# Optimization experiments

Measured on AMD Instinct MI355X. Metric: run time of the kernel, lower is better.

Reference implementation:

```python
import jax, jax.numpy as jnp
import numpy as np

N, E, IN = 90000, 540000, 30
H1, H2, H3, H4 = 128, 128, 128, 64

def _glorot(k, i, o):
    return jax.random.normal(k, (i, o), jnp.float32) * np.float32(np.sqrt(2.0 / (i + o)))

def setup_inputs() -> dict:
    key = jax.random.key(0)
    ks = jax.random.split(key, 20)
    inp = {
        'x': jax.random.normal(ks[0], (N, IN), jnp.float32),
        'edge_index': jax.random.randint(ks[1], (2, E), 0, N, dtype=jnp.int32),
    }
    shapes = [(IN, H1), (H1, H2), (H2, H3), (H3, H4)]
    i = 2
    for br in ('s', 't'):
        for li, (din, dout) in enumerate(shapes, start=1):
            inp[f'w{li}{br}'] = _glorot(ks[i], din, dout); i += 1
            inp[f'b{li}{br}'] = jnp.zeros((dout,), jnp.float32)
    return inp

def _mlp(h, w1, b1, w2, b2):
    # Linear -> (Dropout eval = identity) -> ReLU -> Linear
    return jax.nn.relu(h @ w1 + b1) @ w2 + b2

def _gin(h, src, dst, w1, b1, w2, b2):
    # GINConv with eps=0: MLP(x_i + sum_{j->i} x_j)
    agg = jax.ops.segment_sum(h[src], dst, num_segments=N)
    return _mlp(h + agg, w1, b1, w2, b2)

def reference(x, edge_index, w1s, b1s, w2s, b2s, w3s, b3s, w4s, b4s,
              w1t, b1t, w2t, b2t, w3t, b3t, w4t, b4t):
    src, dst = edge_index[0], edge_index[1]
    z_src = _gin(x, src, dst, w1s, b1s, w2s, b2s)       # [N, H2]
    z_src = _gin(z_src, src, dst, w3s, b3s, w4s, b4s)   # [N, H4]
    z_tar = _gin(x, src, dst, w1t, b1t, w2t, b2t)
    z_tar = _gin(z_tar, src, dst, w3t, b3t, w4t, b4t)
    zs = z_src.reshape(-1, 9, H4)  # [G, 9, H4]
    zt = z_tar.reshape(-1, 9, H4)
    adj = jnp.einsum('gik,gjk->gij', zs, zt)  # per-graph 9x9 matmul
    return adj.reshape(-1, 9)  # [N, 9], matches torch.cat along dim 0
```

## Files before the change

kernel.cpp:

```cpp
#include <hip/hip_runtime.h>
#include <hip/hip_bf16.h>


typedef __attribute__((ext_vector_type(8))) short short8;
typedef __attribute__((ext_vector_type(4))) float f32x4;

#define MAXDEG 64

__device__ inline unsigned short f2bf(float f) {
    union { float f; unsigned u; } v; v.f = f;
    unsigned r = v.u + 0x7fffu + ((v.u >> 16) & 1u);
    return (unsigned short)(r >> 16);
}
__device__ inline float bflo(unsigned u) { return __uint_as_float(u << 16); }
__device__ inline float bfhi(unsigned u) { return __uint_as_float(u & 0xffff0000u); }
__device__ inline unsigned packbf(float a, float b) {
    return (unsigned)f2bf(a) | ((unsigned)f2bf(b) << 16);
}

#define W1S_OFF 0
#define W2S_OFF 4096
#define W3S_OFF 20480
#define W4S_OFF 36864
#define W1T_OFF 45056
#define W2T_OFF 49152
#define W3T_OFF 65536
#define W4T_OFF 81920
#define PACK_USHORTS 90112
#define WPACK_BLOCKS 176

__global__ __launch_bounds__(256) void prep_bucket_kernel(
    const float* w0, const float* w1, const float* w2, const float* w3,
    const float* w4, const float* w5, const float* w6, const float* w7,
    unsigned short* __restrict__ pack,
    const float* __restrict__ x, float* __restrict__ xpad,
    const int* __restrict__ src, const int* __restrict__ dst,
    int* __restrict__ deg, int* __restrict__ colb,
    int N, int E, int nbE)
{
    int bid = blockIdx.x;
    if (bid < nbE) {
        int e = bid * 256 + threadIdx.x;
        if (e < E) {
            int d = dst[e];
            int slot = atomicAdd(&deg[d], 1);
            if (slot < MAXDEG) colb[(size_t)d * MAXDEG + slot] = src[e];
        }
        return;
    }
    bid -= nbE;
    if (bid < WPACK_BLOCKS) {
        if (threadIdx.x >= 64) return;
        const int prefix[9] = {0, 8, 40, 72, 88, 96, 128, 160, 176};
        const int KTa[8] = {1, 4, 4, 4, 1, 4, 4, 4};
        const int KRa[8] = {30, 128, 128, 128, 30, 128, 128, 128};
        const int Ca[8]  = {128, 128, 128, 64, 128, 128, 128, 64};
        const int DOFF[8] = {W1S_OFF, W2S_OFF, W3S_OFF, W4S_OFF,
                             W1T_OFF, W2T_OFF, W3T_OFF, W4T_OFF};
        const float* Ws[8] = {w0, w1, w2, w3, w4, w5, w6, w7};
        int mi = 0;
        while (mi < 7 && bid >= prefix[mi + 1]) ++mi;
        int lt = bid - prefix[mi];
        int kt = lt % KTa[mi], ct = lt / KTa[mi];
        const float* W = Ws[mi];
        int l = threadIdx.x;
        int n = ct * 16 + (l & 15);
        for (int j = 0; j < 8; ++j) {
            int k = kt * 32 + (l >> 4) * 8 + j;
            float v = (k < KRa[mi]) ? W[(size_t)k * Ca[mi] + n] : 0.f;
            pack[(size_t)DOFF[mi] + (size_t)lt * 512 + l * 8 + j] = f2bf(v);
        }
    } else {
        int gid = (bid - WPACK_BLOCKS) * 256 + threadIdx.x;
        if (gid >= N * 32) return;
        int n = gid >> 5, f = gid & 31;
        xpad[gid] = (f < 30) ? x[(size_t)n * 30 + f] : 0.f;
    }
}

__global__ __launch_bounds__(512, 8) void mlp1_kernel(
    const float* __restrict__ xpad, const int* __restrict__ deg,
    const int* __restrict__ colb, const unsigned short* __restrict__ pack,
    const float* __restrict__ b1s, const float* __restrict__ b2s,
    const float* __restrict__ b1t, const float* __restrict__ b2t,
    unsigned short* __restrict__ z1cat, int N)
{
    __shared__ __align__(16) unsigned short hs[64 * 40];
    __shared__ __align__(16) unsigned short hm[2][64 * 136];
    const int tid = threadIdx.x;
    const int n0blk = blockIdx.x * 64;

    {
        const int row = tid >> 3, l = tid & 7;
        int gn = n0blk + row;
        float4 a = {0.f, 0.f, 0.f, 0.f};
        if (gn < N) {
            const float4* base = (const float4*)xpad;
            a = base[(size_t)gn * 8 + l];
            const int* col = colb + (size_t)gn * MAXDEG;
            int e = min(deg[gn], MAXDEG);
            int i = 0;
            for (; i + 4 <= e; i += 4) {
                int s0 = col[i], s1 = col[i + 1], s2 = col[i + 2], s3 = col[i + 3];
                float4 v0 = base[(size_t)s0 * 8 + l];
                float4 v1 = base[(size_t)s1 * 8 + l];
                float4 v2 = base[(size_t)s2 * 8 + l];
                float4 v3 = base[(size_t)s3 * 8 + l];
                a.x += v0.x; a.y += v0.y; a.z += v0.z; a.w += v0.w;
                a.x += v1.x; a.y += v1.y; a.z += v1.z; a.w += v1.w;
                a.x += v2.x; a.y += v2.y; a.z += v2.z; a.w += v2.w;
                a.x += v3.x; a.y += v3.y; a.z += v3.z; a.w += v3.w;
            }
            for (; i + 2 <= e; i += 2) {
                int s0 = col[i], s1 = col[i + 1];
                float4 v0 = base[(size_t)s0 * 8 + l];
                float4 v1 = base[(size_t)s1 * 8 + l];
                a.x += v0.x; a.y += v0.y; a.z += v0.z; a.w += v0.w;
                a.x += v1.x; a.y += v1.y; a.z += v1.z; a.w += v1.w;
            }
            for (; i < e; ++i) {
                float4 v0 = base[(size_t)col[i] * 8 + l];
                a.x += v0.x; a.y += v0.y; a.z += v0.z; a.w += v0.w;
            }
        }
        uint2 o; o.x = packbf(a.x, a.y); o.y = packbf(a.z, a.w);
        *(uint2*)&hs[row * 40 + l * 4] = o;
    }
    __syncthreads();

    const int half = tid >> 8;
    const int ltid = tid & 255;
    const int wv = ltid >> 6, l = ltid & 63, q = l >> 4, m = l & 15;
    const float* B1 = half ? b1t : b1s;
    const float* B2 = half ? b2t : b2s;
    const int w1off = half ? W1T_OFF : W1S_OFF;
    const int w2off = half ? W2T_OFF : W2S_OFF;
    unsigned short* hmb = hm[half];

    {
        short8 a[4];
        #pragma unroll
        for (int nt = 0; nt < 4; ++nt)
            a[nt] = *(const short8*)&hs[(nt * 16 + m) * 40 + q * 8];
        #pragma unroll
        for (int ci = 0; ci < 2; ++ci) {
            int ct = wv * 2 + ci;
            short8 bf = *(const short8*)&pack[w1off + ((size_t)ct * 64 + l) * 8];
            float bias = B1[ct * 16 + m];
            #pragma unroll
            for (int nt = 0; nt < 4; ++nt) {
                f32x4 acc = {0.f, 0.f, 0.f, 0.f};
                acc = __builtin_amdgcn_mfma_f32_16x16x32_bf16(a[nt], bf, acc, 0, 0, 0);
                #pragma unroll
                for (int r = 0; r < 4; ++r) {
                    float v = fmaxf(acc[r] + bias, 0.f);
                    hmb[(nt * 16 + q * 4 + r) * 136 + ct * 16 + m] = f2bf(v);
                }
            }
        }
    }
    __syncthreads();

    f32x4 acc2[4][2];
    #pragma unroll
    for (int nt = 0; nt < 4; ++nt)
        #pragma unroll
        for (int ci = 0; ci < 2; ++ci)
            acc2[nt][ci] = (f32x4){0.f, 0.f, 0.f, 0.f};
    for (int nt = 0; nt < 4; ++nt) {
        short8 a[4];
        #pragma unroll
        for (int kt = 0; kt < 4; ++kt)
            a[kt] = *(const short8*)&hmb[(nt * 16 + m) * 136 + kt * 32 + q * 8];
        #pragma unroll
        for (int ci = 0; ci < 2; ++ci) {
            int ct = wv * 2 + ci;
            #pragma unroll
            for (int kt = 0; kt < 4; ++kt) {
                short8 bf = *(const short8*)&pack[w2off + ((size_t)(ct * 4 + kt) * 64 + l) * 8];
                acc2[nt][ci] = __builtin_amdgcn_mfma_f32_16x16x32_bf16(a[kt], bf, acc2[nt][ci], 0, 0, 0);
            }
        }
    }
    __syncthreads();
    #pragma unroll
    for (int ci = 0; ci < 2; ++ci) {
        int ct = wv * 2 + ci;
        float bias = B2[ct * 16 + m];
        #pragma unroll
        for (int nt = 0; nt < 4; ++nt)
            #pragma unroll
            for (int r = 0; r < 4; ++r)
                hmb[(nt * 16 + q * 4 + r) * 136 + ct * 16 + m] =
                    f2bf(acc2[nt][ci][r] + bias);
    }
    __syncthreads();
    for (int c = tid; c < 2048; c += 512) {
        int row = c >> 5, off = c & 31;
        int gn = n0blk + row;
        if (gn < N) {
            short8 v = *(const short8*)&hm[off >> 4][row * 136 + (off & 15) * 8];
            *(short8*)&z1cat[(size_t)gn * 256 + off * 8] = v;
        }
    }
}

__global__ __launch_bounds__(512, 8) void mlp2_kernel(
    const unsigned short* __restrict__ z1, const int* __restrict__ deg,
    const int* __restrict__ colb, const unsigned short* __restrict__ pack,
    const float* __restrict__ b3s, const float* __restrict__ b4s,
    const float* __restrict__ b3t, const float* __restrict__ b4t,
    float* __restrict__ out, int N, int G)
{
    __shared__ __align__(16) unsigned short hs[36 * 264];
    __shared__ __align__(16) unsigned short hm[36 * 136];
    float* hsf = (float*)hs;
    const int tid = threadIdx.x;
    const int n0blk = blockIdx.x * 36;
    const int wv = tid >> 6, l = tid & 63;

    {
        const uint2* b2 = (const uint2*)z1;
        for (int rr = 0; rr < 5; ++rr) {
            int row = wv + rr * 8;
            if (row >= 36) break;
            int gn = n0blk + row;
            float a0 = 0.f, a1 = 0.f, a2 = 0.f, a3 = 0.f;
            if (gn < N) {
                uint2 s = b2[(size_t)gn * 64 + l];
                a0 = bflo(s.x); a1 = bfhi(s.x); a2 = bflo(s.y); a3 = bfhi(s.y);
                const int* col = colb + (size_t)gn * MAXDEG;
                int e = min(deg[gn], MAXDEG);
                #pragma unroll
                for (int i = 0; i < 8; ++i) {
                    int valid = i < e;
                    int s0 = valid ? col[i] : gn;
                    float fv = valid ? 1.f : 0.f;
                    uint2 v = b2[(size_t)s0 * 64 + l];
                    a0 = fmaf(fv, bflo(v.x), a0);
                    a1 = fmaf(fv, bfhi(v.x), a1);
                    a2 = fmaf(fv, bflo(v.y), a2);
                    a3 = fmaf(fv, bfhi(v.y), a3);
                }
                int i = 8;
                for (; i + 4 <= e; i += 4) {
                    int s0 = col[i], s1 = col[i + 1], s2 = col[i + 2], s3 = col[i + 3];
                    uint2 v0 = b2[(size_t)s0 * 64 + l];
                    uint2 v1 = b2[(size_t)s1 * 64 + l];
                    uint2 v2 = b2[(size_t)s2 * 64 + l];
                    uint2 v3 = b2[(size_t)s3 * 64 + l];
                    a0 += bflo(v0.x); a1 += bfhi(v0.x); a2 += bflo(v0.y); a3 += bfhi(v0.y);
                    a0 += bflo(v1.x); a1 += bfhi(v1.x); a2 += bflo(v1.y); a3 += bfhi(v1.y);
                    a0 += bflo(v2.x); a1 += bfhi(v2.x); a2 += bflo(v2.y); a3 += bfhi(v2.y);
                    a0 += bflo(v3.x); a1 += bfhi(v3.x); a2 += bflo(v3.y); a3 += bfhi(v3.y);
                }
                for (; i < e; ++i) {
                    uint2 v0 = b2[(size_t)col[i] * 64 + l];
                    a0 += bflo(v0.x); a1 += bfhi(v0.x); a2 += bflo(v0.y); a3 += bfhi(v0.y);
                }
            }
            uint2 o; o.x = packbf(a0, a1); o.y = packbf(a2, a3);
            *(uint2*)&hs[row * 264 + l * 4] = o;
        }
    }
    __syncthreads();

    const int q = l >> 4, m = l & 15;

    for (int br = 0; br < 2; ++br) {
        const int w1off = br ? W3T_OFF : W3S_OFF;
        const int w2off = br ? W4T_OFF : W4S_OFF;
        const float* B1 = br ? b3t : b3s;
        const float* B2 = br ? b4t : b4s;
        if (br) __syncthreads();

        #pragma unroll
        for (int ti = 0; ti < 3; ++ti) {
            const int tile = wv * 3 + ti;
            const int ct = tile & 7;
            const int nt = tile >> 3;
            const int ar = min(nt * 16 + m, 35);
            float bias = B1[ct * 16 + m];
            short8 a[4];
            #pragma unroll
            for (int kt = 0; kt < 4; ++kt)
                a[kt] = *(const short8*)&hs[ar * 264 + br * 128 + kt * 32 + q * 8];
            f32x4 acc = {0.f, 0.f, 0.f, 0.f};
            #pragma unroll
            for (int kt = 0; kt < 4; ++kt) {
                short8 bf = *(const short8*)&pack[w1off + ((size_t)(ct * 4 + kt) * 64 + l) * 8];
                acc = __builtin_amdgcn_mfma_f32_16x16x32_bf16(a[kt], bf, acc, 0, 0, 0);
            }
            #pragma unroll
            for (int r = 0; r < 4; ++r) {
                int hrow = nt * 16 + q * 4 + r;
                if (hrow < 36) {
                    float v = fmaxf(acc[r] + bias, 0.f);
                    hm[hrow * 136 + ct * 16 + m] = f2bf(v);
                }
            }
        }
        __syncthreads();

        #pragma unroll
        for (int ti = 0; ti < 2; ++ti) {
            const int tile = ti * 8 + wv;
            if (tile < 12) {
                const int ct = tile & 3;
                const int nt = tile >> 2;
                const int ar = min(nt * 16 + m, 35);
                float bias = B2[ct * 16 + m];
                short8 a[4];
                #pragma unroll
                for (int kt = 0; kt < 4; ++kt)
                    a[kt] = *(const short8*)&hm[ar * 136 + kt * 32 + q * 8];
                f32x4 acc = {0.f, 0.f, 0.f, 0.f};
                #pragma unroll
                for (int kt = 0; kt < 4; ++kt) {
                    short8 bf = *(const short8*)&pack[w2off + ((size_t)(ct * 4 + kt) * 64 + l) * 8];
                    acc = __builtin_amdgcn_mfma_f32_16x16x32_bf16(a[kt], bf, acc, 0, 0, 0);
                }
                #pragma unroll
                for (int r = 0; r < 4; ++r) {
                    int zrow = nt * 16 + q * 4 + r;
                    if (zrow < 36)
                        hsf[zrow * 132 + br * 64 + ct * 16 + m] = acc[r] + bias;
                }
            }
        }
    }
    __syncthreads();

    if (tid < 324) {
        int gl = tid / 81, rem = tid - gl * 81;
        int i = rem / 9, j = rem - i * 9;
        int g = blockIdx.x * 4 + gl;
        if (g < G) {
            const float* srow = &hsf[(gl * 9 + i) * 132];
            const float* trow = &hsf[(gl * 9 + j) * 132 + 64];
            float acc = 0.f;
            #pragma unroll
            for (int k = 0; k < 64; ++k) acc += srow[k] * trow[k];
            out[(size_t)g * 81 + i * 9 + j] = acc;
        }
    }
}

extern "C" void kernel_launch(void* const* d_in, const int* in_sizes, int n_in,
                              void* d_out, int out_size, void* d_ws, size_t ws_size,
                              hipStream_t stream)
{
    const float* x  = (const float*)d_in[0];
    const int*   ei = (const int*)d_in[1];
    const int N_ = in_sizes[0] / 30;
    const int E_ = in_sizes[1] / 2;
    const int* src = ei;
    const int* dst = ei + E_;

    const float* w1s = (const float*)d_in[2];
    const float* b1s = (const float*)d_in[3];
    const float* w2s = (const float*)d_in[4];
    const float* b2s = (const float*)d_in[5];
    const float* w3s = (const float*)d_in[6];
    const float* b3s = (const float*)d_in[7];
    const float* w4s = (const float*)d_in[8];
    const float* b4s = (const float*)d_in[9];
    const float* w1t = (const float*)d_in[10];
    const float* b1t = (const float*)d_in[11];
    const float* w2t = (const float*)d_in[12];
    const float* b2t = (const float*)d_in[13];
    const float* w3t = (const float*)d_in[14];
    const float* b3t = (const float*)d_in[15];
    const float* w4t = (const float*)d_in[16];
    const float* b4t = (const float*)d_in[17];

    int* deg  = (int*)d_ws;
    int* colb = deg + N_;
    size_t int_bytes = ((size_t)N_ * (1 + MAXDEG)) * sizeof(int);
    size_t pb = (int_bytes + 15) & ~(size_t)15;
    unsigned short* packu = (unsigned short*)((char*)d_ws + pb);
    float* xpad = (float*)(packu + PACK_USHORTS);
    unsigned short* z1cat = (unsigned short*)(xpad + (size_t)N_ * 32);
    size_t need = pb + (size_t)PACK_USHORTS * 2
                + (size_t)N_ * 32 * 4
                + (size_t)N_ * 256 * 2;
    if (ws_size < need) return;

    const int nbE  = (E_ + 255) / 256;
    const int nb64 = (N_ + 63) / 64;
    const int nb36 = (N_ + 35) / 36;
    const int nbX  = (N_ * 32 + 255) / 256;

    hipMemsetAsync(deg, 0, (size_t)N_ * sizeof(int), stream);

    prep_bucket_kernel<<<nbE + WPACK_BLOCKS + nbX, 256, 0, stream>>>(
        w1s, w2s, w3s, w4s, w1t, w2t, w3t, w4t, packu, x, xpad,
        src, dst, deg, colb, N_, E_, nbE);

    mlp1_kernel<<<nb64, 512, 0, stream>>>(xpad, deg, colb, packu,
        b1s, b2s, b1t, b2t, z1cat, N_);

    mlp2_kernel<<<nb36, 512, 0, stream>>>(z1cat, deg, colb, packu,
        b3s, b4s, b3t, b4t, (float*)d_out, N_, N_ / 9);
}
```

Baseline: 248.1 us.

## Stage neighbor row gathers through LDS with double-buffered async global_load_lds

Replaces the per-lane register gather of neighbor feature rows in the second-layer aggregation with a double-buffered staging scheme. Each wave fetches four neighbor rows at a time directly into a private LDS slice with global_load_lds, prefetching the next chunk while summing the current one. The staging area is carved out of an enlarged shared buffer that also hosts the hm array, so per-block LDS grows and occupancy may drop. The code has no explicit wait on the async copies before reading LDS, so correctness relies on waits the compiler inserts.

```diff
diff --git a/kernel.cpp b/kernel.cpp
--- a/kernel.cpp
+++ b/kernel.cpp
@@ -212,14 +212,18 @@
     const float* __restrict__ b3t, const float* __restrict__ b4t,
     float* __restrict__ out, int N, int G)
 {
-    __shared__ __align__(16) unsigned short hs[36 * 264];
-    __shared__ __align__(16) unsigned short hm[36 * 136];
-    float* hsf = (float*)hs;
+    __shared__ __align__(16) unsigned char smem[19008 + 32768];
+    unsigned short* hs = (unsigned short*)smem;
+    unsigned short* hm = (unsigned short*)(smem + 19008);
+    unsigned char*  stg = smem + 19008;
+    float* hsf = (float*)smem;
     const int tid = threadIdx.x;
     const int n0blk = blockIdx.x * 36;
     const int wv = tid >> 6, l = tid & 63;
 
     {
+        unsigned char* mystg = stg + wv * 4096;
+        const int hl = l >> 5, ll = l & 31;
         const uint2* b2 = (const uint2*)z1;
         for (int rr = 0; rr < 5; ++rr) {
             int row = wv + rr * 8;
@@ -231,32 +235,43 @@
                 a0 = bflo(s.x); a1 = bfhi(s.x); a2 = bflo(s.y); a3 = bfhi(s.y);
                 const int* col = colb + (size_t)gn * MAXDEG;
                 int e = min(deg[gn], MAXDEG);
-                #pragma unroll
-                for (int i = 0; i < 8; ++i) {
-                    int valid = i < e;
-                    int s0 = valid ? col[i] : gn;
-                    float fv = valid ? 1.f : 0.f;
-                    uint2 v = b2[(size_t)s0 * 64 + l];
-                    a0 = fmaf(fv, bflo(v.x), a0);
-                    a1 = fmaf(fv, bfhi(v.x), a1);
-                    a2 = fmaf(fv, bflo(v.y), a2);
-                    a3 = fmaf(fv, bfhi(v.y), a3);
-                }
-                int i = 8;
-                for (; i + 4 <= e; i += 4) {
-                    int s0 = col[i], s1 = col[i + 1], s2 = col[i + 2], s3 = col[i + 3];
-                    uint2 v0 = b2[(size_t)s0 * 64 + l];
-                    uint2 v1 = b2[(size_t)s1 * 64 + l];
-                    uint2 v2 = b2[(size_t)s2 * 64 + l];
-                    uint2 v3 = b2[(size_t)s3 * 64 + l];
-                    a0 += bflo(v0.x); a1 += bfhi(v0.x); a2 += bflo(v0.y); a3 += bfhi(v0.y);
-                    a0 += bflo(v1.x); a1 += bfhi(v1.x); a2 += bflo(v1.y); a3 += bfhi(v1.y);
-                    a0 += bflo(v2.x); a1 += bfhi(v2.x); a2 += bflo(v2.y); a3 += bfhi(v2.y);
-                    a0 += bflo(v3.x); a1 += bfhi(v3.x); a2 += bflo(v3.y); a3 += bfhi(v3.y);
-                }
-                for (; i < e; ++i) {
-                    uint2 v0 = b2[(size_t)col[i] * 64 + l];
-                    a0 += bflo(v0.x); a1 += bfhi(v0.x); a2 += bflo(v0.y); a3 += bfhi(v0.y);
+                int nch = (e + 3) >> 2;
+                if (nch > 0) {
+                    {
+                        int jA = min(0 + hl, e - 1);
+                        int jB = min(2 + hl, e - 1);
+                        const char* gA = (const char*)z1 + (size_t)col[jA] * 512 + ll * 16;
+                        const char* gB = (const char*)z1 + (size_t)col[jB] * 512 + ll * 16;
+                        __builtin_amdgcn_global_load_lds(
+                            (const __attribute__((address_space(1))) void*)gA,
+                            (__attribute__((address_space(3))) void*)mystg, 16, 0, 0);
+                        __builtin_amdgcn_global_load_lds(
+                            (const __attribute__((address_space(1))) void*)gB,
+                            (__attribute__((address_space(3))) void*)(mystg + 1024), 16, 0, 0);
+                    }
+                    for (int k = 0; k < nch; ++k) {
+                        if (k + 1 < nch) {
+                            unsigned char* nbuf = mystg + ((k + 1) & 1) * 2048;
+                            int j0 = (k + 1) * 4;
+                            int jA = min(j0 + hl, e - 1);
+                            int jB = min(j0 + 2 + hl, e - 1);
+                            const char* gA = (const char*)z1 + (size_t)col[jA] * 512 + ll * 16;
+                            const char* gB = (const char*)z1 + (size_t)col[jB] * 512 + ll * 16;
+                            __builtin_amdgcn_global_load_lds(
+                                (const __attribute__((address_space(1))) void*)gA,
+                                (__attribute__((address_space(3))) void*)nbuf, 16, 0, 0);
+                            __builtin_amdgcn_global_load_lds(
+                                (const __attribute__((address_space(1))) void*)gB,
+                                (__attribute__((address_space(3))) void*)(nbuf + 1024), 16, 0, 0);
+                        }
+                        const unsigned char* buf = mystg + (k & 1) * 2048;
+                        int jmax = min(4, e - k * 4);
+                        for (int j = 0; j < jmax; ++j) {
+                            uint2 v = *(const uint2*)(buf + j * 512 + (size_t)l * 8);
+                            a0 += bflo(v.x); a1 += bfhi(v.x);
+                            a2 += bflo(v.y); a3 += bfhi(v.y);
+                        }
+                    }
                 }
             }
             uint2 o; o.x = packbf(a0, a1); o.y = packbf(a2, a3);
```

Result: faster. 240.9 us (-2.9%).
